# Kernel tuning notes

Measured on AMD Instinct MI355X. Metric: run time of the kernel, lower is better.

Reference implementation:

```python
import jax, jax.numpy as jnp
import numpy as np
from jax import lax

EPS = 1e-5
N_WIRES, N_LAYERS = 4, 3
DIM = 2 ** N_WIRES  # 16

# Static CNOT permutations for control w, target w+1 (state @ CNOT => new[k] = old[k ^ (((k>>c)&1)<<t)])
_idx = np.arange(DIM)
CNOT_PERMS = [jnp.asarray(_idx ^ (((_idx >> w) & 1) << (w + 1))) for w in range(N_WIRES - 1)]


def conv3x3(x, w):
    # x: [B,1,H,W], w: [1,1,3,3], padding=1, no bias
    return lax.conv_general_dilated(x, w, (1, 1), 'SAME',
                                    dimension_numbers=('NCHW', 'OIHW', 'NCHW'))


def batchnorm_train(x, gamma, beta):
    # training-mode BN: batch statistics over (B,H,W), biased variance
    mean = jnp.mean(x, axis=(0, 2, 3), keepdims=True)
    var = jnp.var(x, axis=(0, 2, 3), keepdims=True)
    xn = (x - mean) * lax.rsqrt(var + EPS)
    return xn * gamma.reshape(1, -1, 1, 1) + beta.reshape(1, -1, 1, 1)


def residual_block(x, w1, g1, b1, w2, g2, b2):
    out = jax.nn.relu(batchnorm_train(conv3x3(x, w1), g1, b1))
    out = batchnorm_train(conv3x3(out, w2), g2, b2)
    return jax.nn.relu(out + x)


def quantum_feat4(theta):
    # Faithful to QuantumKernel: real state, each RZ scales by cos(theta/2)
    # (rz[0,0]==rz[1,1]==cos(theta/2)), CNOT is a bit-indexed permutation.
    # State is independent of the patch values (patch is never used).
    s = jnp.zeros(DIM, dtype=theta.dtype).at[0].set(1.0)
    for l in range(N_LAYERS):
        s = s * jnp.prod(jnp.cos(theta[l] / 2.0))  # 8 RZ scalings for this layer
        for w in range(N_WIRES - 1):
            s = s[CNOT_PERMS[w]]
    probs = s ** 2
    return probs[:4]


def setup_inputs() -> dict:
    key = jax.random.key(0)
    ks = jax.random.split(key, 12)
    B = 16384
    d = dict(
        x=jax.random.normal(ks[0], (B, 1, 28, 28), dtype=jnp.float32),
        theta=jax.random.normal(ks[1], (N_LAYERS, N_WIRES, 2), dtype=jnp.float32),
        r1_w1=jax.random.normal(ks[2], (1, 1, 3, 3), dtype=jnp.float32) * 0.3,
        r1_g1=jnp.ones((1,), jnp.float32), r1_b1=jnp.zeros((1,), jnp.float32),
        r1_w2=jax.random.normal(ks[3], (1, 1, 3, 3), dtype=jnp.float32) * 0.3,
        r1_g2=jnp.ones((1,), jnp.float32), r1_b2=jnp.zeros((1,), jnp.float32),
        r2_w1=jax.random.normal(ks[4], (1, 1, 3, 3), dtype=jnp.float32) * 0.3,
        r2_g1=jnp.ones((1,), jnp.float32), r2_b1=jnp.zeros((1,), jnp.float32),
        r2_w2=jax.random.normal(ks[5], (1, 1, 3, 3), dtype=jnp.float32) * 0.3,
        r2_g2=jnp.ones((1,), jnp.float32), r2_b2=jnp.zeros((1,), jnp.float32),
        fc_w=jax.random.normal(ks[6], (10, 784), dtype=jnp.float32) * 0.03,
        fc_b=jnp.zeros((10,), jnp.float32),
        alpha=jnp.asarray(0.5, dtype=jnp.float32),
    )
    return d


def reference(x, theta, r1_w1, r1_g1, r1_b1, r1_w2, r1_g2, r1_b2,
              r2_w1, r2_g1, r2_b1, r2_w2, r2_g2, r2_b2, fc_w, fc_b, alpha):
    B = x.shape[0]
    cls_feat = residual_block(x, r1_w1, r1_g1, r1_b1, r1_w2, r1_g2, r1_b2)
    cls_feat = residual_block(cls_feat, r2_w1, r2_g1, r2_b1, r2_w2, r2_g2, r2_b2)
    cls_flat = cls_feat.reshape(B, -1)  # [B, 784]

    # Quantum filter: kernel output ignores patch values, identical for all
    # 196 patches and all batch elements; cat along dim=1 -> tile the 4-vector.
    p4 = quantum_feat4(theta)                           # [4]
    q_feat = jnp.broadcast_to(jnp.tile(p4, 14 * 14), (B, 784))

    fused = alpha * cls_flat + (1.0 - alpha) * q_feat
    logits = fused @ fc_w.T + fc_b
    return jax.nn.log_softmax(logits, axis=-1)
```

## Files before the change

### kernel.cpp

```cpp
#include <hip/hip_runtime.h>
#include <hip/hip_fp16.h>
#include <math.h>

#define BATCH   16384
#define IMGPIX  784
#define NTOT    (BATCH * IMGPIX)
#define NSLOT   64
#define SLOTSTR 8
#define STAGE_DBL (NSLOT * SLOTSTR)
#define TROW 224
#define TGRP 6272
#define CONVBLK 3584

typedef _Float16 half8 __attribute__((ext_vector_type(8)));
typedef float f32x4 __attribute__((ext_vector_type(4)));

struct __align__(8) h4 { __half2 lo, hi; };
__device__ __forceinline__ h4 f4_to_h4(float4 v) {
    h4 r; r.lo = __floats2half2_rn(v.x, v.y); r.hi = __floats2half2_rn(v.z, v.w); return r;
}
__device__ __forceinline__ float4 h4_to_f4(h4 p) {
    float2 a = __half22float2(p.lo), b = __half22float2(p.hi);
    return make_float4(a.x, a.y, b.x, b.y);
}
#define ZERO4 make_float4(0.f, 0.f, 0.f, 0.f)

__device__ __forceinline__ void block_stats_atomic(double lsum, double lsq, double* slot) {
    __shared__ double red[4][2];
    #pragma unroll
    for (int off = 32; off >= 1; off >>= 1) {
        lsum += __shfl_down(lsum, off, 64);
        lsq  += __shfl_down(lsq,  off, 64);
    }
    const int lane = threadIdx.x & 63;
    const int w    = threadIdx.x >> 6;
    if (lane == 0) { red[w][0] = lsum; red[w][1] = lsq; }
    __syncthreads();
    if (threadIdx.x == 0) {
        double ts = (red[0][0] + red[1][0]) + (red[2][0] + red[3][0]);
        double tq = (red[0][1] + red[1][1]) + (red[2][1] + red[3][1]);
        atomicAdd(&slot[0], ts);
        atomicAdd(&slot[1], tq);
    }
}

__device__ __forceinline__ float2 stats_ab(const double* __restrict__ stats_in,
                                           float gamma, float beta) {
    int lane = threadIdx.x & 63;
    double s = stats_in[lane * SLOTSTR];
    double q = stats_in[lane * SLOTSTR + 1];
    #pragma unroll
    for (int off = 32; off >= 1; off >>= 1) {
        s += __shfl_down(s, off, 64);
        q += __shfl_down(q, off, 64);
    }
    s = __shfl(s, 0, 64);
    q = __shfl(q, 0, 64);
    const double INV_N = 1.0 / (double)NTOT;
    double mean = s * INV_N;
    double var  = q * INV_N - mean * mean;
    float rstd = 1.0f / sqrtf((float)var + 1e-5f);
    float a  = gamma * rstd;
    float bb = beta - (float)mean * a;
    return make_float2(a, bb);
}

__device__ __forceinline__ float4 hrow(float wl, float wc, float wr,
                                       float L, float4 v, float R) {
    float4 h;
    h.x = fmaf(wl, L,   fmaf(wc, v.x, wr * v.y));
    h.y = fmaf(wl, v.x, fmaf(wc, v.y, wr * v.z));
    h.z = fmaf(wl, v.y, fmaf(wc, v.z, wr * v.w));
    h.w = fmaf(wl, v.z, fmaf(wc, v.w, wr * R));
    return h;
}

__device__ __forceinline__ void emit_row(__half* dst, int r, float4 o, float mf,
                                         double& lsum, double& lsq, bool act) {
    if (act) *(h4*)(dst + r * TROW) = f4_to_h4(o);
    float s4 = (o.x + o.y) + (o.z + o.w);
    float q4 = fmaf(o.x, o.x, fmaf(o.y, o.y, fmaf(o.z, o.z, o.w * o.w)));
    lsum += (double)(mf * s4);
    lsq  += (double)(mf * q4);
}

#define LANE_SETUP()                                                          \
    const int t = threadIdx.x;                                                \
    const int lane = t & 63;                                                  \
    const int widx = t >> 6;                                                  \
    const int c4   = lane & 7;                                                \
    const bool act = (c4 < 7);                                                \
    const float mf = act ? 1.f : 0.f;                                         \
    const int c4c  = c4 < 7 ? c4 : 6;                                         \
    const int task = blockIdx.x * 4 + widx;                     \
    const int s    = task >> 11;                              \
    const int G    = task & 2047;                          \
    const int r0   = s * 4;                                                   \
    const int rtop = (r0 > 0)  ? (r0 - 1) : 0;                                \
    const int rbot = (r0 < 24) ? (r0 + 4) : 27;                               \
    const int i8   = lane >> 3;                                               \
    const int img  = G * 8 + i8;                                              \
    const size_t xbase = (size_t)img * IMGPIX + c4c * 4;                      \
    const size_t tbR   = (size_t)G * TGRP + c4c * 32 + i8 * 4;                \
    const size_t tbW   = (size_t)G * TGRP + c4  * 32 + i8 * 4;

#define CONV_STEP(k, v)                                                       \
    {                                                                         \
        float L = __shfl_up((v).w, 1, 64);  if (c4 == 0) L = 0.f;             \
        float R = __shfl_down((v).x, 1, 64); if (c4 == 6) R = 0.f;            \
        float4 h2 = hrow(w9[6], w9[7], w9[8], L, (v), R);                     \
        float4 h1 = hrow(w9[3], w9[4], w9[5], L, (v), R);                     \
        float4 h0 = hrow(w9[0], w9[1], w9[2], L, (v), R);                     \
        accA.x += h2.x; accA.y += h2.y; accA.z += h2.z; accA.w += h2.w;       \
        if ((k) >= 2) emit_row(dst, r0 + (k) - 2, accA, mf, lsum, lsq, act);  \
        accA.x = accB.x + h1.x; accA.y = accB.y + h1.y;                       \
        accA.z = accB.z + h1.z; accA.w = accB.w + h1.w;                       \
        accB = h0;                                                            \
    }

#define HALO_ZERO(k, v)                                                       \
    if ((k) == 0 && r0 == 0)  (v) = ZERO4;                                    \
    if ((k) == 5 && r0 == 24) (v) = ZERO4;

__global__ __launch_bounds__(256, 2) void k_conv_plain(const float* __restrict__ in,
        const float* __restrict__ w, __half* __restrict__ out,
        __half* __restrict__ x16_out, double* __restrict__ stats_out,
        const float* __restrict__ fc_w, const float* __restrict__ fc_b,
        const float* __restrict__ theta, const float* __restrict__ alpha_p,
        __half* __restrict__ Bpack, float* __restrict__ qkpad)
{
    LANE_SETUP();
    float w9[9];
    #pragma unroll
    for (int i = 0; i < 9; i++) w9[i] = w[i];
    const float* src = in + xbase;
    __half* dst  = out + tbW;
    __half* dstx = x16_out + tbW;

    float4 vb[6];
    vb[0] = *(const float4*)(src + rtop * 28);
    #pragma unroll
    for (int k = 1; k < 5; k++) vb[k] = *(const float4*)(src + (r0 - 1 + k) * 28);
    vb[5] = *(const float4*)(src + rbot * 28);
    __builtin_amdgcn_sched_barrier(0);

    float4 accA = ZERO4, accB = ZERO4;
    double lsum = 0.0, lsq = 0.0;
    #pragma unroll
    for (int k = 0; k < 6; k++) {
        float4 v = vb[k];
        if (act && k >= 1 && k <= 4)
            *(h4*)(dstx + (r0 - 1 + k) * TROW) = f4_to_h4(vb[k]);
        HALO_ZERO(k, v);
        CONV_STEP(k, v);
    }
    block_stats_atomic(lsum, lsq, &stats_out[(blockIdx.x & (NSLOT - 1)) * SLOTSTR]);

    if (blockIdx.x < 56) {
        const int idx = blockIdx.x * 256 + t;
        const int r = idx >> 9;
        const int l = (idx >> 3) & 63;
        const int j = idx & 7;
        const int n = l & 15;
        const int c = ((l >> 4) << 3) + j;
        float v = 0.f;
        if (c < 28 && n < 10) v = fc_w[n * 784 + r * 28 + c];
        Bpack[idx] = __float2half(v);
    } else if (blockIdx.x == 56) {
        __shared__ float csum[10];
        if (t < 80) {
            int k = t >> 3, oct = t & 7;
            float sm = 0.f;
            #pragma unroll
            for (int i = 0; i < 25; i++) {
                int p = oct + 8 * i;
                if (p < 196) sm += fc_w[k * 784 + p * 4];
            }
            sm += __shfl_xor(sm, 1, 64);
            sm += __shfl_xor(sm, 2, 64);
            sm += __shfl_xor(sm, 4, 64);
            if (oct == 0) csum[k] = sm;
        }
        __syncthreads();
        if (t < 16) {
            float val = -1e30f;
            if (t < 10) {
                float c = 1.f;
                #pragma unroll
                for (int i = 0; i < 24; i++) c *= cosf(theta[i] * 0.5f);
                val = fmaf((1.f - alpha_p[0]) * c * c, csum[t], fc_b[t]);
            }
            qkpad[t] = val;
        }
    }
}

__global__ __launch_bounds__(256, 8) void k_conv_affine(const __half* __restrict__ in,
        const double* __restrict__ stats_in,
        const float* __restrict__ gamma, const float* __restrict__ beta,
        const float* __restrict__ w, __half* __restrict__ out, double* __restrict__ stats_out)
{
    LANE_SETUP();
    float2 ab = stats_ab(stats_in, gamma[0], beta[0]);
    float w9[9];
    #pragma unroll
    for (int i = 0; i < 9; i++) w9[i] = w[i];
    const __half* src = in + tbR;
    __half* dst = out + tbW;

    h4 vb[6];
    vb[0] = *(const h4*)(src + rtop * TROW);
    #pragma unroll
    for (int k = 1; k < 5; k++) vb[k] = *(const h4*)(src + (r0 - 1 + k) * TROW);
    vb[5] = *(const h4*)(src + rbot * TROW);
    __builtin_amdgcn_sched_barrier(0);

    float4 accA = ZERO4, accB = ZERO4;
    double lsum = 0.0, lsq = 0.0;
    #pragma unroll
    for (int k = 0; k < 6; k++) {
        float4 r4 = h4_to_f4(vb[k]);
        float4 v;
        v.x = fmaxf(fmaf(ab.x, r4.x, ab.y), 0.f);
        v.y = fmaxf(fmaf(ab.x, r4.y, ab.y), 0.f);
        v.z = fmaxf(fmaf(ab.x, r4.z, ab.y), 0.f);
        v.w = fmaxf(fmaf(ab.x, r4.w, ab.y), 0.f);
        HALO_ZERO(k, v);
        CONV_STEP(k, v);
    }
    block_stats_atomic(lsum, lsq, &stats_out[(blockIdx.x & (NSLOT - 1)) * SLOTSTR]);
}

__global__ __launch_bounds__(256, 8) void k_conv_resid(const __half* __restrict__ y2,
        const __half* __restrict__ x16, const double* __restrict__ stats_in,
        const float* __restrict__ gamma, const float* __restrict__ beta,
        const float* __restrict__ w, __half* __restrict__ y3_out,
        __half* __restrict__ o1_out, double* __restrict__ stats_out)
{
    LANE_SETUP();
    float2 ab = stats_ab(stats_in, gamma[0], beta[0]);
    float w9[9];
    #pragma unroll
    for (int i = 0; i < 9; i++) w9[i] = w[i];
    const __half* srcy = y2 + tbR;
    const __half* srcx = x16 + tbR;
    __half* dst  = y3_out + tbW;
    __half* dsto = o1_out + tbW;

    h4 yb[6], xb[6];
    yb[0] = *(const h4*)(srcy + rtop * TROW);
    xb[0] = *(const h4*)(srcx + rtop * TROW);
    #pragma unroll
    for (int k = 1; k < 5; k++) {
        yb[k] = *(const h4*)(srcy + (r0 - 1 + k) * TROW);
        xb[k] = *(const h4*)(srcx + (r0 - 1 + k) * TROW);
    }
    yb[5] = *(const h4*)(srcy + rbot * TROW);
    xb[5] = *(const h4*)(srcx + rbot * TROW);
    __builtin_amdgcn_sched_barrier(0);

    float4 accA = ZERO4, accB = ZERO4;
    double lsum = 0.0, lsq = 0.0;
    #pragma unroll
    for (int k = 0; k < 6; k++) {
        float4 r4 = h4_to_f4(yb[k]);
        float4 x4 = h4_to_f4(xb[k]);
        float4 v;
        v.x = fmaxf(fmaf(ab.x, r4.x, ab.y) + x4.x, 0.f);
        v.y = fmaxf(fmaf(ab.x, r4.y, ab.y) + x4.y, 0.f);
        v.z = fmaxf(fmaf(ab.x, r4.z, ab.y) + x4.z, 0.f);
        v.w = fmaxf(fmaf(ab.x, r4.w, ab.y) + x4.w, 0.f);
        HALO_ZERO(k, v);
        if (act && k >= 1 && k <= 4)
            *(h4*)(dsto + (r0 - 1 + k) * TROW) = f4_to_h4(v);
        CONV_STEP(k, v);
    }
    block_stats_atomic(lsum, lsq, &stats_out[(blockIdx.x & (NSLOT - 1)) * SLOTSTR]);
}

__global__ __launch_bounds__(256, 4) void k_head_mfma(const __half* __restrict__ y4,
        const __half* __restrict__ o1, const double* __restrict__ stats_in,
        const float* __restrict__ gamma, const float* __restrict__ beta,
        const __half* __restrict__ Bpack, const float* __restrict__ qkpad,
        const float* __restrict__ alpha_p, float* __restrict__ out)
{
    __shared__ float accs[4][64][4];
    const int t    = threadIdx.x;
    const int lane = t & 63;
    const int q    = t >> 6;
    float2 ab = stats_ab(stats_in, gamma[0], beta[0]);

    const int m   = lane & 15;
    const int jg  = lane >> 4;
    const int c4a = jg * 2;
    const int c4b = (jg == 3) ? 6 : (jg * 2 + 1);
    const int G   = blockIdx.x * 2 + (m >> 3);
    const int i8  = m & 7;
    const size_t base = (size_t)G * TGRP + i8 * 4;
    const __half* ya = y4 + base;
    const __half* oa = o1 + base;

    f32x4 acc = {0.f, 0.f, 0.f, 0.f};
    #pragma unroll
    for (int rr = 0; rr < 7; rr++) {
        const int r  = q * 7 + rr;
        const int ro = r * TROW;
        h4 ylo = *(const h4*)(ya + ro + c4a * 32);
        h4 yhi = *(const h4*)(ya + ro + c4b * 32);
        h4 olo = *(const h4*)(oa + ro + c4a * 32);
        h4 ohi = *(const h4*)(oa + ro + c4b * 32);
        float4 yf0 = h4_to_f4(ylo), yf1 = h4_to_f4(yhi);
        float4 of0 = h4_to_f4(olo), of1 = h4_to_f4(ohi);
        float4 va, vb;
        va.x = fmaxf(fmaf(ab.x, yf0.x, ab.y) + of0.x, 0.f);
        va.y = fmaxf(fmaf(ab.x, yf0.y, ab.y) + of0.y, 0.f);
        va.z = fmaxf(fmaf(ab.x, yf0.z, ab.y) + of0.z, 0.f);
        va.w = fmaxf(fmaf(ab.x, yf0.w, ab.y) + of0.w, 0.f);
        vb.x = fmaxf(fmaf(ab.x, yf1.x, ab.y) + of1.x, 0.f);
        vb.y = fmaxf(fmaf(ab.x, yf1.y, ab.y) + of1.y, 0.f);
        vb.z = fmaxf(fmaf(ab.x, yf1.z, ab.y) + of1.z, 0.f);
        vb.w = fmaxf(fmaf(ab.x, yf1.w, ab.y) + of1.w, 0.f);
        union { half8 v; h4 qq[2]; } A;
        A.qq[0] = f4_to_h4(va);
        A.qq[1] = f4_to_h4(vb);
        half8 B = *(const half8*)(Bpack + (r * 64 + lane) * 8);
        acc = __builtin_amdgcn_mfma_f32_16x16x32_f16(A.v, B, acc, 0, 0, 0);
    }
    #pragma unroll
    for (int i = 0; i < 4; i++) accs[q][lane][i] = acc[i];
    __syncthreads();

    if (t < 64) {
        float c[4];
        #pragma unroll
        for (int i = 0; i < 4; i++)
            c[i] = (accs[0][lane][i] + accs[1][lane][i])
                 + (accs[2][lane][i] + accs[3][lane][i]);
        const float alpha = alpha_p[0];
        const int cls = lane & 15;
        const float qv = qkpad[cls];
        #pragma unroll
        for (int i = 0; i < 4; i++) {
            float logit = fmaf(alpha, c[i], qv);
            float mx = logit;
            mx = fmaxf(mx, __shfl_xor(mx, 1, 64));
            mx = fmaxf(mx, __shfl_xor(mx, 2, 64));
            mx = fmaxf(mx, __shfl_xor(mx, 4, 64));
            mx = fmaxf(mx, __shfl_xor(mx, 8, 64));
            float se = __expf(logit - mx);
            se += __shfl_xor(se, 1, 64);
            se += __shfl_xor(se, 2, 64);
            se += __shfl_xor(se, 4, 64);
            se += __shfl_xor(se, 8, 64);
            float lse = mx + __logf(se);
            if (cls < 10) {
                int img = blockIdx.x * 16 + (lane >> 4) * 4 + i;
                out[(size_t)img * 10 + cls] = logit - lse;
            }
        }
    }
}

extern "C" void kernel_launch(void* const* d_in, const int* in_sizes, int n_in,
                              void* d_out, int out_size, void* d_ws, size_t ws_size,
                              hipStream_t stream) {
    const float* x     = (const float*)d_in[0];
    const float* theta = (const float*)d_in[1];
    const float* r1_w1 = (const float*)d_in[2];
    const float* r1_g1 = (const float*)d_in[3];
    const float* r1_b1 = (const float*)d_in[4];
    const float* r1_w2 = (const float*)d_in[5];
    const float* r1_g2 = (const float*)d_in[6];
    const float* r1_b2 = (const float*)d_in[7];
    const float* r2_w1 = (const float*)d_in[8];
    const float* r2_g1 = (const float*)d_in[9];
    const float* r2_b1 = (const float*)d_in[10];
    const float* r2_w2 = (const float*)d_in[11];
    const float* r2_g2 = (const float*)d_in[12];
    const float* r2_b2 = (const float*)d_in[13];
    const float* fc_w  = (const float*)d_in[14];
    const float* fc_b  = (const float*)d_in[15];
    const float* alpha = (const float*)d_in[16];
    float* out = (float*)d_out;

    double* stats = (double*)d_ws;
    float*  qkpad = (float*)((char*)d_ws + 16384);
    __half* Bpack = (__half*)((char*)d_ws + 16448);
    __half* bufA  = (__half*)((char*)d_ws + 65536);
    __half* bufB  = bufA + (size_t)NTOT;
    __half* bufD  = bufB + (size_t)NTOT;
    __half* bufX  = bufD + (size_t)NTOT;

    double* s_y1 = stats + 0 * STAGE_DBL;
    double* s_y2 = stats + 1 * STAGE_DBL;
    double* s_y3 = stats + 2 * STAGE_DBL;
    double* s_y4 = stats + 3 * STAGE_DBL;

    hipMemsetAsync(stats, 0, 4 * STAGE_DBL * sizeof(double), stream);
    k_conv_plain<<<CONVBLK, 256, 0, stream>>>(x, r1_w1, bufA, bufX, s_y1,
                                              fc_w, fc_b, theta, alpha,
                                              Bpack, qkpad);
    k_conv_affine<<<CONVBLK, 256, 0, stream>>>(bufA, s_y1, r1_g1, r1_b1, r1_w2, bufB, s_y2);
    k_conv_resid<<<CONVBLK, 256, 0, stream>>>(bufB, bufX, s_y2, r1_g2, r1_b2, r2_w1, bufA, bufD, s_y3);
    k_conv_affine<<<CONVBLK, 256, 0, stream>>>(bufA, s_y3, r2_g1, r2_b1, r2_w2, bufB, s_y4);
    k_head_mfma<<<1024, 256, 0, stream>>>(bufB, bufD, s_y4, r2_g2, r2_b2,
                                          Bpack, qkpad, alpha, out);
}
```

Baseline: 88.35 us.

## Make first conv waves loop over all row strips with prefetch

The first conv kernel now assigns one wave per 8-image group and loops over all seven 4-row strips. It prefetches the next strip's input rows into registers while computing the current one, replacing the old scheme of one strip per wave. The grid shrinks from 3584 to 512 blocks and launch bounds allow four blocks per CU. This cuts per-block launch and setup overhead and overlaps loads with compute, but leaves far fewer waves in flight to hide memory latency. It also serializes each wave's work, so the extra tail duties in blocks 0–56 finish later.

New measurement: 95.62 us. +8.2%, slower.

```diff
diff --git a/kernel.cpp b/kernel.cpp
--- a/kernel.cpp
+++ b/kernel.cpp
@@ -99,8 +99,6 @@
     const int rtop = (r0 > 0)  ? (r0 - 1) : 0;                                \
     const int rbot = (r0 < 24) ? (r0 + 4) : 27;                               \
     const int i8   = lane >> 3;                                               \
-    const int img  = G * 8 + i8;                                              \
-    const size_t xbase = (size_t)img * IMGPIX + c4c * 4;                      \
     const size_t tbR   = (size_t)G * TGRP + c4c * 32 + i8 * 4;                \
     const size_t tbW   = (size_t)G * TGRP + c4  * 32 + i8 * 4;
 
@@ -122,39 +120,63 @@
     if ((k) == 0 && r0 == 0)  (v) = ZERO4;                                    \
     if ((k) == 5 && r0 == 24) (v) = ZERO4;
 
-__global__ __launch_bounds__(256, 2) void k_conv_plain(const float* __restrict__ in,
+__global__ __launch_bounds__(256, 4) void k_conv_plain(const float* __restrict__ in,
         const float* __restrict__ w, __half* __restrict__ out,
         __half* __restrict__ x16_out, double* __restrict__ stats_out,
         const float* __restrict__ fc_w, const float* __restrict__ fc_b,
         const float* __restrict__ theta, const float* __restrict__ alpha_p,
         __half* __restrict__ Bpack, float* __restrict__ qkpad)
 {
-    LANE_SETUP();
+    const int t    = threadIdx.x;
+    const int lane = t & 63;
+    const int widx = t >> 6;
+    const int c4   = lane & 7;
+    const bool act = (c4 < 7);
+    const float mf = act ? 1.f : 0.f;
+    const int c4c  = c4 < 7 ? c4 : 6;
+    const int i8   = lane >> 3;
+    const int G    = blockIdx.x * 4 + widx;
+    const int img  = G * 8 + i8;
+    const float* src = in + (size_t)img * IMGPIX + c4c * 4;
+    __half* dst  = out     + (size_t)G * TGRP + c4 * 32 + i8 * 4;
+    __half* dstx = x16_out + (size_t)G * TGRP + c4 * 32 + i8 * 4;
+
     float w9[9];
     #pragma unroll
     for (int i = 0; i < 9; i++) w9[i] = w[i];
-    const float* src = in + xbase;
-    __half* dst  = out + tbW;
-    __half* dstx = x16_out + tbW;
-
-    float4 vb[6];
-    vb[0] = *(const float4*)(src + rtop * 28);
-    #pragma unroll
-    for (int k = 1; k < 5; k++) vb[k] = *(const float4*)(src + (r0 - 1 + k) * 28);
-    vb[5] = *(const float4*)(src + rbot * 28);
-    __builtin_amdgcn_sched_barrier(0);
-
-    float4 accA = ZERO4, accB = ZERO4;
+
+    float4 cur[6], nxt[6];
+    cur[0] = *(const float4*)(src);
+    #pragma unroll
+    for (int k = 1; k < 5; k++) cur[k] = *(const float4*)(src + (k - 1) * 28);
+    cur[5] = *(const float4*)(src + 4 * 28);
+
     double lsum = 0.0, lsq = 0.0;
     #pragma unroll
-    for (int k = 0; k < 6; k++) {
-        float4 v = vb[k];
-        if (act && k >= 1 && k <= 4)
-            *(h4*)(dstx + (r0 - 1 + k) * TROW) = f4_to_h4(vb[k]);
-        HALO_ZERO(k, v);
-        CONV_STEP(k, v);
-    }
-    block_stats_atomic(lsum, lsq, &stats_out[(blockIdx.x & (NSLOT - 1)) * SLOTSTR]);
+    for (int s = 0; s < 7; s++) {
+        const int r0 = s * 4;
+        if (s < 6) {
+            const int rtn = r0 + 3;
+            const int rbn = (r0 + 4 < 24) ? (r0 + 8) : 27;
+            nxt[0] = *(const float4*)(src + rtn * 28);
+            #pragma unroll
+            for (int k = 1; k < 5; k++)
+                nxt[k] = *(const float4*)(src + (rtn + k) * 28);
+            nxt[5] = *(const float4*)(src + rbn * 28);
+        }
+        float4 accA = ZERO4, accB = ZERO4;
+        #pragma unroll
+        for (int k = 0; k < 6; k++) {
+            float4 v = cur[k];
+            if (act && k >= 1 && k <= 4)
+                *(h4*)(dstx + (r0 - 1 + k) * TROW) = f4_to_h4(cur[k]);
+            HALO_ZERO(k, v);
+            CONV_STEP(k, v);
+        }
+        #pragma unroll
+        for (int k = 0; k < 6; k++) cur[k] = nxt[k];
+    }
+    block_stats_atomic(lsum, lsq, &stats_out[(G & (NSLOT - 1)) * SLOTSTR]);
 
     if (blockIdx.x < 56) {
         const int idx = blockIdx.x * 256 + t;
@@ -397,9 +419,9 @@
     double* s_y4 = stats + 3 * STAGE_DBL;
 
     hipMemsetAsync(stats, 0, 4 * STAGE_DBL * sizeof(double), stream);
-    k_conv_plain<<<CONVBLK, 256, 0, stream>>>(x, r1_w1, bufA, bufX, s_y1,
-                                              fc_w, fc_b, theta, alpha,
-                                              Bpack, qkpad);
+    k_conv_plain<<<512, 256, 0, stream>>>(x, r1_w1, bufA, bufX, s_y1,
+                                          fc_w, fc_b, theta, alpha,
+                                          Bpack, qkpad);
     k_conv_affine<<<CONVBLK, 256, 0, stream>>>(bufA, s_y1, r1_g1, r1_b1, r1_w2, bufB, s_y2);
     k_conv_resid<<<CONVBLK, 256, 0, stream>>>(bufB, bufX, s_y2, r1_g2, r1_b2, r2_w1, bufA, bufD, s_y3);
     k_conv_affine<<<CONVBLK, 256, 0, stream>>>(bufA, s_y3, r2_g1, r2_b1, r2_w2, bufB, s_y4);
```
